# Kernel optimization log

Hardware: AMD Instinct MI355X
Metric: run time of the kernel (lower is better)

Reference implementation:

```python
import jax, jax.numpy as jnp
import numpy as np

NEG_SLOPE = 0.2
EPS = 1e-16


def glorot(key, shape):
    fan = shape[0] + shape[-1] if len(shape) == 2 else shape[-1] * 2
    lim = jnp.sqrt(6.0 / fan)
    return jax.random.uniform(key, shape, minval=-lim, maxval=lim, dtype=jnp.float32)


def setup_inputs() -> dict:
    key = jax.random.key(0)
    ks = jax.random.split(key, 16)
    B, N, E = 4, 50000, 800000
    F_in, H, C, n_cls = 128, 4, 16, 16
    x = jax.random.normal(ks[0], (B, N, F_in), dtype=jnp.float32)
    edge_index = jax.random.randint(ks[1], (2, E), 0, N, dtype=jnp.int64)
    inp = {
        "x": x,
        "edge_index": edge_index,
        # layer 1: 128 -> 4 heads x 16, concat
        "W1": glorot(ks[2], (F_in, H * C)),
        "a1s": glorot(ks[3], (H, C)),
        "a1d": glorot(ks[4], (H, C)),
        "b1": jnp.zeros((H * C,), jnp.float32),
        # layer 2: 64 -> 4 heads x 16, concat
        "W2": glorot(ks[5], (H * C, H * C)),
        "a2s": glorot(ks[6], (H, C)),
        "a2d": glorot(ks[7], (H, C)),
        "b2": jnp.zeros((H * C,), jnp.float32),
        # layer 3: 64 -> 1 head x num_classes, concat
        "W3": glorot(ks[8], (H * C, n_cls)),
        "a3s": glorot(ks[9], (1, n_cls)),
        "a3d": glorot(ks[10], (1, n_cls)),
        "b3": jnp.zeros((n_cls,), jnp.float32),
    }
    return inp


def gat_conv(x, W, a_src, a_dst, b, src, dst, N, concat):
    # x: [N, F_in]; W: [F_in, H*C]
    H, C = a_src.shape
    h = (x @ W).reshape(N, H, C)
    e_src = jnp.einsum('nhc,hc->nh', h, a_src)  # [N, H]
    e_dst = jnp.einsum('nhc,hc->nh', h, a_dst)  # [N, H]
    e = jax.nn.leaky_relu(e_src[src] + e_dst[dst], NEG_SLOPE)  # [E, H]
    # segment softmax over incoming edges of each target node
    m = jax.ops.segment_max(e, dst, num_segments=N)  # [N, H]
    ex = jnp.exp(e - m[dst])
    denom = jax.ops.segment_sum(ex, dst, num_segments=N)  # [N, H]
    alpha = ex / (denom[dst] + EPS)  # [E, H]
    out = jax.ops.segment_sum(alpha[:, :, None] * h[src], dst, num_segments=N)  # [N, H, C]
    out = out.reshape(N, H * C) if concat else out.mean(axis=1)
    return out + b


def reference(x, edge_index, W1, a1s, a1d, b1, W2, a2s, a2d, b2, W3, a3s, a3d, b3):
    B, N, _ = x.shape
    # add self-loops (PyG GATConv default)
    loop = jnp.arange(N, dtype=edge_index.dtype)
    src = jnp.concatenate([edge_index[0], loop])
    dst = jnp.concatenate([edge_index[1], loop])

    def fwd_single(xi):
        h = jax.nn.relu(gat_conv(xi, W1, a1s, a1d, b1, src, dst, N, True))
        h = jax.nn.relu(gat_conv(h, W2, a2s, a2d, b2, src, dst, N, True))
        return gat_conv(h, W3, a3s, a3d, b3, src, dst, N, True)

    return jax.vmap(fwd_single)(x)  # [B, N, num_classes]
```

## Files before the change

kernel.cpp:

```cpp
#include <hip/hip_runtime.h>
#include <hip/hip_bf16.h>
#include <hip/hip_fp16.h>
#include <math.h>


#define NEG_SLOPE 0.2f

constexpr int NN   = 50000;
constexpr int FIN  = 128;
constexpr int HC   = 64;
constexpr int NCLS = 16;

typedef _Float16 half4 __attribute__((ext_vector_type(4)));
typedef float    f32x4 __attribute__((ext_vector_type(4)));

struct H16 { __half2 h[8]; };


__global__ void init_deg_kernel(int* deg, int N) {
    int t = blockIdx.x * blockDim.x + threadIdx.x;
    if (t < N) deg[t] = 1;
}

__global__ void hist_kernel(const int* __restrict__ ei, int* deg, int E) {
    int t = blockIdx.x * blockDim.x + threadIdx.x;
    if (t < E) atomicAdd(&deg[ei[E + t]], 1);
}

__global__ __launch_bounds__(1024) void scan1_kernel(
    const int* __restrict__ deg, int* __restrict__ rp,
    int* __restrict__ bsum, int N) {
    __shared__ int buf[1024];
    int i = blockIdx.x * 1024 + threadIdx.x;
    int v = (i < N) ? deg[i] : 0;
    buf[threadIdx.x] = v;
    __syncthreads();
#pragma unroll
    for (int off = 1; off < 1024; off <<= 1) {
        int t = (threadIdx.x >= (unsigned)off) ? buf[threadIdx.x - off] : 0;
        __syncthreads();
        buf[threadIdx.x] += t;
        __syncthreads();
    }
    if (i < N) rp[i] = buf[threadIdx.x] - v;
    if (threadIdx.x == 1023) bsum[blockIdx.x] = buf[1023];
}

__global__ void scan2_kernel(int* __restrict__ bsum, int nb,
                             int* __restrict__ rp, int N) {
    int lane = threadIdx.x;
    int v = (lane < nb) ? bsum[lane] : 0;
#pragma unroll
    for (int off = 1; off < 64; off <<= 1) {
        int t = __shfl_up(v, off);
        if (lane >= off) v += t;
    }
    if (lane < nb) bsum[lane] = v;
    if (lane == nb - 1) rp[N] = v;
}

__global__ __launch_bounds__(1024) void scan3_kernel(
    int* __restrict__ rp, int* __restrict__ wp,
    const int* __restrict__ bsum, int N) {
    int i = blockIdx.x * 1024 + threadIdx.x;
    if (i >= N) return;
    int add = (blockIdx.x > 0) ? bsum[blockIdx.x - 1] : 0;
    int r = rp[i] + add;
    rp[i] = r;
    wp[i] = r;
}

__global__ void scatter_kernel(const int* __restrict__ ei, int* wp,
                               int* __restrict__ col, int E, int N) {
    int t = blockIdx.x * blockDim.x + threadIdx.x;
    int total = E + N;
    if (t >= total) return;
    if (t < E) {
        int s = ei[t];
        int d = ei[E + t];
        int pos = atomicAdd(&wp[d], 1);
        col[pos] = s;
    } else {
        int n = t - E;
        int pos = atomicAdd(&wp[n], 1);
        col[pos] = n;
    }
}


__global__ void prep_w_kernel(const float* __restrict__ W1,
                              const float* __restrict__ W2,
                              const float* __restrict__ W3,
                              __half* __restrict__ Wt1,
                              __half* __restrict__ Wt2,
                              __half* __restrict__ Wt3) {
    int t = blockIdx.x * 256 + threadIdx.x;
    if (t < 64 * 128) { int c = t >> 7, k = t & 127; Wt1[t] = __float2half(W1[k * 64 + c]); }
    if (t < 64 * 64)  { int c = t >> 6, k = t & 63;  Wt2[t] = __float2half(W2[k * 64 + c]); }
    if (t < 16 * 64)  { int c = t >> 6, k = t & 63;  Wt3[t] = __float2half(W3[k * 16 + c]); }
}


template <int K, int M, int BF, bool IN16>
__global__ __launch_bounds__(256) void gemm_mfma_kernel(
    const void* __restrict__ Xin, const __half* __restrict__ Wt_g,
    const float* __restrict__ as_, const float* __restrict__ ad_,
    __half* __restrict__ Hout, float* __restrict__ Es, float* __restrict__ Ed,
    int N) {
    constexpr int CT = M / 16;
    constexpr int PK = K + 8;
    constexpr int KS = K / 16;
    __shared__ _Float16 Xs[64 * PK];
    __shared__ _Float16 Ws[M * PK];
    const int b = blockIdx.y;
    const int t = threadIdx.x;
    const int node00 = blockIdx.x * 64;

    {
        const float4* wsrc = reinterpret_cast<const float4*>(Wt_g);
        constexpr int WC8 = K / 8;
        for (int idx = t; idx < M * WC8; idx += 256) {
            int c = idx / WC8, kk = idx - c * WC8;
            *reinterpret_cast<float4*>(&Ws[c * PK + kk * 8]) = wsrc[idx];
        }
    }
    if (IN16) {
        const __half* Xh = (const __half*)Xin;
        constexpr int C8 = K / 8;
        for (int idx = t; idx < 64 * C8; idx += 256) {
            int row = idx / C8, k8 = idx - row * C8;
            int node = node00 + row;
            if (node >= N) node = N - 1;
            const float4* src = reinterpret_cast<const float4*>(
                Xh + ((size_t)node * BF + b) * K + k8 * 8);
            *reinterpret_cast<float4*>(&Xs[row * PK + k8 * 8]) = *src;
        }
    } else {
        const float* Xf = (const float*)Xin;
        constexpr int C4 = K / 4;
        for (int idx = t; idx < 64 * C4; idx += 256) {
            int row = idx / C4, k4 = idx - row * C4;
            int node = node00 + row;
            if (node >= N) node = N - 1;
            float4 xv = *reinterpret_cast<const float4*>(
                Xf + ((size_t)b * N + node) * K + k4 * 4);
            half4 hv;
            hv[0] = (_Float16)xv.x; hv[1] = (_Float16)xv.y;
            hv[2] = (_Float16)xv.z; hv[3] = (_Float16)xv.w;
            *reinterpret_cast<half4*>(&Xs[row * PK + k4 * 4]) = hv;
        }
    }
    __syncthreads();

    const int lane = t & 63;
    const int w    = t >> 6;
    const int l15  = lane & 15;
    const int lg   = lane >> 4;
    const int rowb = w * 16;

    f32x4 acc[CT];
#pragma unroll
    for (int ct = 0; ct < CT; ++ct)
#pragma unroll
        for (int r = 0; r < 4; ++r) acc[ct][r] = 0.f;

#pragma unroll
    for (int ks = 0; ks < KS; ++ks) {
        half4 a = *reinterpret_cast<const half4*>(
            &Xs[(rowb + l15) * PK + ks * 16 + lg * 4]);
#pragma unroll
        for (int ct = 0; ct < CT; ++ct) {
            half4 bf = *reinterpret_cast<const half4*>(
                &Ws[(ct * 16 + l15) * PK + ks * 16 + lg * 4]);
            acc[ct] = __builtin_amdgcn_mfma_f32_16x16x16f16(a, bf, acc[ct], 0, 0, 0);
        }
    }

    _Float16* Hh = reinterpret_cast<_Float16*>(Hout);
#pragma unroll
    for (int ct = 0; ct < CT; ++ct) {
        float a_s = as_[ct * 16 + l15];
        float a_d = ad_[ct * 16 + l15];
#pragma unroll
        for (int r = 0; r < 4; ++r) {
            int node = node00 + rowb + lg * 4 + r;
            float hv = acc[ct][r];
            float ps = hv * a_s, pd = hv * a_d;
            ps += __shfl_xor(ps, 1); ps += __shfl_xor(ps, 2);
            ps += __shfl_xor(ps, 4); ps += __shfl_xor(ps, 8);
            pd += __shfl_xor(pd, 1); pd += __shfl_xor(pd, 2);
            pd += __shfl_xor(pd, 4); pd += __shfl_xor(pd, 8);
            if (node < N) {
                Hh[((size_t)node * BF + b) * M + ct * 16 + l15] = (_Float16)hv;
                if (l15 == 0) {
                    Es[((size_t)node * BF + b) * CT + ct] = ps;
                    Ed[((size_t)node * BF + b) * CT + ct] = pd;
                }
            }
        }
    }
}


template <int H, bool RELU, bool OUTB, bool OUTH, int BF>
__global__ __launch_bounds__(256) void agg_kernel(
    const int* __restrict__ rp, const int* __restrict__ col,
    const __half* __restrict__ Hm, const float* __restrict__ Es,
    const float* __restrict__ Ed, const float* __restrict__ bias,
    void* __restrict__ Out, int N) {
    constexpr int C = 16;
    constexpr int M = H * C;
    int t = blockIdx.x * 256 + threadIdx.x;
    if (t >= N * H * BF) return;
    int u = t;
    const int b  = u % BF; u /= BF;
    const int hd = u % H;  u /= H;
    const int n  = u;

    const float ed = Ed[((size_t)n * BF + b) * H + hd];
    const int beg = rp[n], end = rp[n + 1];

    float m = -1e30f, dn = 0.f;
    float acc[C];
#pragma unroll
    for (int j = 0; j < C; ++j) acc[j] = 0.f;

    int i = beg;
    int sA = col[i];
    float esA = Es[((size_t)sA * BF + b) * H + hd];
    H16 hA = *reinterpret_cast<const H16*>(Hm + ((size_t)sA * BF + b) * M + hd * C);

    while (true) {
        int inext = i + 1;
        bool more = (inext < end);
        int sB = 0; float esB = 0.f; H16 hB;
        if (more) {
            sB = col[inext];
            esB = Es[((size_t)sB * BF + b) * H + hd];
            hB = *reinterpret_cast<const H16*>(Hm + ((size_t)sB * BF + b) * M + hd * C);
        }

        float e = esA + ed;
        e = (e >= 0.f) ? e : NEG_SLOPE * e;
        float2 f0 = __half22float2(hA.h[0]);
        float2 f1 = __half22float2(hA.h[1]);
        float2 f2 = __half22float2(hA.h[2]);
        float2 f3 = __half22float2(hA.h[3]);
        float2 f4 = __half22float2(hA.h[4]);
        float2 f5 = __half22float2(hA.h[5]);
        float2 f6 = __half22float2(hA.h[6]);
        float2 f7 = __half22float2(hA.h[7]);
        if (e > m) {
            float sc = __expf(m - e);
            m = e;
            dn = fmaf(dn, sc, 1.0f);
            acc[0]=fmaf(acc[0],sc,f0.x);   acc[1]=fmaf(acc[1],sc,f0.y);
            acc[2]=fmaf(acc[2],sc,f1.x);   acc[3]=fmaf(acc[3],sc,f1.y);
            acc[4]=fmaf(acc[4],sc,f2.x);   acc[5]=fmaf(acc[5],sc,f2.y);
            acc[6]=fmaf(acc[6],sc,f3.x);   acc[7]=fmaf(acc[7],sc,f3.y);
            acc[8]=fmaf(acc[8],sc,f4.x);   acc[9]=fmaf(acc[9],sc,f4.y);
            acc[10]=fmaf(acc[10],sc,f5.x); acc[11]=fmaf(acc[11],sc,f5.y);
            acc[12]=fmaf(acc[12],sc,f6.x); acc[13]=fmaf(acc[13],sc,f6.y);
            acc[14]=fmaf(acc[14],sc,f7.x); acc[15]=fmaf(acc[15],sc,f7.y);
        } else {
            float ex = __expf(e - m);
            dn += ex;
            acc[0]=fmaf(ex,f0.x,acc[0]);   acc[1]=fmaf(ex,f0.y,acc[1]);
            acc[2]=fmaf(ex,f1.x,acc[2]);   acc[3]=fmaf(ex,f1.y,acc[3]);
            acc[4]=fmaf(ex,f2.x,acc[4]);   acc[5]=fmaf(ex,f2.y,acc[5]);
            acc[6]=fmaf(ex,f3.x,acc[6]);   acc[7]=fmaf(ex,f3.y,acc[7]);
            acc[8]=fmaf(ex,f4.x,acc[8]);   acc[9]=fmaf(ex,f4.y,acc[9]);
            acc[10]=fmaf(ex,f5.x,acc[10]); acc[11]=fmaf(ex,f5.y,acc[11]);
            acc[12]=fmaf(ex,f6.x,acc[12]); acc[13]=fmaf(ex,f6.y,acc[13]);
            acc[14]=fmaf(ex,f7.x,acc[14]); acc[15]=fmaf(ex,f7.y,acc[15]);
        }
        if (!more) break;
        i = inext; sA = sB; esA = esB; hA = hB;
    }

    float inv = 1.f / (dn + 1e-16f);
    const float* bp = bias + hd * C;
    float vb[C];
#pragma unroll
    for (int j = 0; j < C; ++j) {
        float v = fmaf(acc[j], inv, bp[j]);
        if (RELU) v = fmaxf(v, 0.f);
        vb[j] = v;
    }
    if (OUTH) {
        __half* op = (__half*)Out + ((size_t)n * BF + b) * M + hd * C;
        H16 hv;
#pragma unroll
        for (int j = 0; j < 8; ++j)
            hv.h[j] = __float22half2_rn(make_float2(vb[2 * j], vb[2 * j + 1]));
        *reinterpret_cast<H16*>(op) = hv;
    } else {
        float* op = OUTB ? ((float*)Out + ((size_t)b * N + n) * M + hd * C)
                         : ((float*)Out + ((size_t)n * BF + b) * M + hd * C);
        *reinterpret_cast<float4*>(op + 0)  = make_float4(vb[0], vb[1], vb[2], vb[3]);
        *reinterpret_cast<float4*>(op + 4)  = make_float4(vb[4], vb[5], vb[6], vb[7]);
        *reinterpret_cast<float4*>(op + 8)  = make_float4(vb[8], vb[9], vb[10], vb[11]);
        *reinterpret_cast<float4*>(op + 12) = make_float4(vb[12], vb[13], vb[14], vb[15]);
    }
}


extern "C" void kernel_launch(void* const* d_in, const int* in_sizes, int n_in,
                              void* d_out, int out_size, void* d_ws, size_t ws_size,
                              hipStream_t stream) {
    const float* x   = (const float*)d_in[0];
    const int*   ei  = (const int*)d_in[1];
    const float* W1  = (const float*)d_in[2];
    const float* a1s = (const float*)d_in[3];
    const float* a1d = (const float*)d_in[4];
    const float* b1  = (const float*)d_in[5];
    const float* W2  = (const float*)d_in[6];
    const float* a2s = (const float*)d_in[7];
    const float* a2d = (const float*)d_in[8];
    const float* b2  = (const float*)d_in[9];
    const float* W3  = (const float*)d_in[10];
    const float* a3s = (const float*)d_in[11];
    const float* a3d = (const float*)d_in[12];
    const float* b3  = (const float*)d_in[13];
    float* outp = (float*)d_out;

    const int N  = NN;
    const int E  = in_sizes[1] / 2;
    const int ET = E + N;
    const int B  = in_sizes[0] / (N * FIN);
    const int NB1024 = (N + 1023) / 1024;

    char* ws = (char*)d_ws;
    size_t off = 0;
    auto alloc = [&](size_t bytes) -> void* {
        void* p = ws + off;
        off += (bytes + 255) & ~(size_t)255;
        return p;
    };
    int* deg  = (int*)alloc((size_t)N * 4);
    int* rp   = (int*)alloc((size_t)(N + 1) * 4);
    int* wp   = (int*)alloc((size_t)N * 4);
    int* bsum = (int*)alloc(64 * 4);
    int* col  = (int*)alloc((size_t)ET * 4);
    __half* Wt1 = (__half*)alloc(64 * 128 * 2);
    __half* Wt2 = (__half*)alloc(64 * 64 * 2);
    __half* Wt3 = (__half*)alloc(16 * 64 * 2);

    size_t fused_need = off + 2 * ((size_t)N * B * HC * 2 + 256)
                            + 2 * ((size_t)N * B * 4 * 4 + 256);
    bool fused = (B == 4) && (ws_size >= fused_need);
    int BF = fused ? 4 : 1;

    __half* h  = (__half*)alloc((size_t)N * BF * HC * 2);
    __half* z  = (__half*)alloc((size_t)N * BF * HC * 2);
    float* es  = (float*)alloc((size_t)N * BF * 4 * 4);
    float* edv = (float*)alloc((size_t)N * BF * 4 * 4);

    init_deg_kernel<<<(N + 255) / 256, 256, 0, stream>>>(deg, N);
    hist_kernel<<<(E + 255) / 256, 256, 0, stream>>>(ei, deg, E);
    scan1_kernel<<<NB1024, 1024, 0, stream>>>(deg, rp, bsum, N);
    scan2_kernel<<<1, 64, 0, stream>>>(bsum, NB1024, rp, N);
    scan3_kernel<<<NB1024, 1024, 0, stream>>>(rp, wp, bsum, N);
    scatter_kernel<<<(ET + 255) / 256, 256, 0, stream>>>(ei, wp, col, E, N);
    prep_w_kernel<<<32, 256, 0, stream>>>(W1, W2, W3, Wt1, Wt2, Wt3);

    if (fused) {
        dim3 g((N + 63) / 64, 4);
        int agg12 = (N * 4 * 4 + 255) / 256;
        int agg3  = (N * 4 + 255) / 256;
        gemm_mfma_kernel<128, 64, 4, false><<<g, 256, 0, stream>>>(x, Wt1, a1s, a1d, h, es, edv, N);
        agg_kernel<4, true, false, true, 4><<<agg12, 256, 0, stream>>>(rp, col, h, es, edv, b1, z, N);
        gemm_mfma_kernel<64, 64, 4, true><<<g, 256, 0, stream>>>(z, Wt2, a2s, a2d, h, es, edv, N);
        agg_kernel<4, true, false, true, 4><<<agg12, 256, 0, stream>>>(rp, col, h, es, edv, b2, z, N);
        gemm_mfma_kernel<64, 16, 4, true><<<g, 256, 0, stream>>>(z, Wt3, a3s, a3d, h, es, edv, N);
        agg_kernel<1, false, true, false, 4><<<agg3, 256, 0, stream>>>(rp, col, h, es, edv, b3, outp, N);
    } else {
        dim3 g((N + 63) / 64, 1);
        int agg12 = (N * 4 + 255) / 256;
        int agg3  = (N + 255) / 256;
        for (int b = 0; b < B; ++b) {
            const float* xb = x + (size_t)b * N * FIN;
            float* outb = outp + (size_t)b * N * NCLS;
            gemm_mfma_kernel<128, 64, 1, false><<<g, 256, 0, stream>>>(xb, Wt1, a1s, a1d, h, es, edv, N);
            agg_kernel<4, true, false, true, 1><<<agg12, 256, 0, stream>>>(rp, col, h, es, edv, b1, z, N);
            gemm_mfma_kernel<64, 64, 1, true><<<g, 256, 0, stream>>>(z, Wt2, a2s, a2d, h, es, edv, N);
            agg_kernel<4, true, false, true, 1><<<agg12, 256, 0, stream>>>(rp, col, h, es, edv, b2, z, N);
            gemm_mfma_kernel<64, 16, 1, true><<<g, 256, 0, stream>>>(z, Wt3, a3s, a3d, h, es, edv, N);
            agg_kernel<1, false, false, false, 1><<<agg3, 256, 0, stream>>>(rp, col, h, es, edv, b3, outb, N);
        }
    }
}
```

Measured before the change: 542.1 us.

## Switch to batch-major layout and split aggregation into 4-channel threads

Intermediate buffers move from node-interleaved batch layout to batch-major layout, so the batch index becomes the outermost dimension. The aggregation kernel now assigns each thread 4 channels of a head instead of all 16, giving 4x more threads, with consecutive threads covering adjacent channel chunks of the same node. Gathers within a batch then touch a smaller working set per batch slice and coalesce across the channel chunks. In exchange, each edge's column index, source score and exp are recomputed by four threads, and cache locality across batches for the same node is lost.

```diff
diff --git a/kernel.cpp b/kernel.cpp
--- a/kernel.cpp
+++ b/kernel.cpp
@@ -14,7 +14,7 @@
 typedef _Float16 half4 __attribute__((ext_vector_type(4)));
 typedef float    f32x4 __attribute__((ext_vector_type(4)));
 
-struct H16 { __half2 h[8]; };
+struct H4v { __half2 h[2]; };
 
 
 __global__ void init_deg_kernel(int* deg, int N) {
@@ -101,7 +101,7 @@
 }
 
 
-template <int K, int M, int BF, bool IN16>
+template <int K, int M, bool IN16>
 __global__ __launch_bounds__(256) void gemm_mfma_kernel(
     const void* __restrict__ Xin, const __half* __restrict__ Wt_g,
     const float* __restrict__ as_, const float* __restrict__ ad_,
@@ -132,7 +132,7 @@
             int node = node00 + row;
             if (node >= N) node = N - 1;
             const float4* src = reinterpret_cast<const float4*>(
-                Xh + ((size_t)node * BF + b) * K + k8 * 8);
+                Xh + ((size_t)b * N + node) * K + k8 * 8);
             *reinterpret_cast<float4*>(&Xs[row * PK + k8 * 8]) = *src;
         }
     } else {
@@ -191,10 +191,10 @@
             pd += __shfl_xor(pd, 1); pd += __shfl_xor(pd, 2);
             pd += __shfl_xor(pd, 4); pd += __shfl_xor(pd, 8);
             if (node < N) {
-                Hh[((size_t)node * BF + b) * M + ct * 16 + l15] = (_Float16)hv;
+                Hh[((size_t)b * N + node) * M + ct * 16 + l15] = (_Float16)hv;
                 if (l15 == 0) {
-                    Es[((size_t)node * BF + b) * CT + ct] = ps;
-                    Ed[((size_t)node * BF + b) * CT + ct] = pd;
+                    Es[((size_t)b * N + node) * CT + ct] = ps;
+                    Ed[((size_t)b * N + node) * CT + ct] = pd;
                 }
             }
         }
@@ -202,105 +202,94 @@
 }
 
 
-template <int H, bool RELU, bool OUTB, bool OUTH, int BF>
+template <int H, bool RELU, bool OUTH, int BF>
 __global__ __launch_bounds__(256) void agg_kernel(
     const int* __restrict__ rp, const int* __restrict__ col,
     const __half* __restrict__ Hm, const float* __restrict__ Es,
     const float* __restrict__ Ed, const float* __restrict__ bias,
     void* __restrict__ Out, int N) {
-    constexpr int C = 16;
-    constexpr int M = H * C;
-    int t = blockIdx.x * 256 + threadIdx.x;
-    if (t >= N * H * BF) return;
-    int u = t;
-    const int b  = u % BF; u /= BF;
-    const int hd = u % H;  u /= H;
-    const int n  = u;
-
-    const float ed = Ed[((size_t)n * BF + b) * H + hd];
+    constexpr int M = H * 16;
+    int g = blockIdx.x * 256 + threadIdx.x;
+    int n, b, hd, ch;
+    if (H == 4) {
+        if (g >= N * 16 * BF) return;
+        b = (BF > 1) ? g / (N * 16) : 0;
+        int r = (BF > 1) ? g % (N * 16) : g;
+        n = r >> 4;
+        int q = r & 15;
+        hd = q >> 2;
+        ch = q & 3;
+    } else {
+        if (g >= N * 4 * BF) return;
+        n = g / (4 * BF);
+        int q = g % (4 * BF);
+        b = (BF > 1) ? (q >> 2) : 0;
+        ch = q & 3;
+        hd = 0;
+    }
+    const int c0 = hd * 16 + ch * 4;
+    const size_t tb = (size_t)b * N;
+
+    const float ed = Ed[(tb + n) * H + hd];
     const int beg = rp[n], end = rp[n + 1];
 
     float m = -1e30f, dn = 0.f;
-    float acc[C];
-#pragma unroll
-    for (int j = 0; j < C; ++j) acc[j] = 0.f;
+    float a0 = 0.f, a1 = 0.f, a2 = 0.f, a3 = 0.f;
 
     int i = beg;
     int sA = col[i];
-    float esA = Es[((size_t)sA * BF + b) * H + hd];
-    H16 hA = *reinterpret_cast<const H16*>(Hm + ((size_t)sA * BF + b) * M + hd * C);
+    float esA = Es[(tb + sA) * H + hd];
+    H4v hA = *reinterpret_cast<const H4v*>(Hm + (tb + sA) * M + c0);
 
     while (true) {
         int inext = i + 1;
         bool more = (inext < end);
-        int sB = 0; float esB = 0.f; H16 hB;
+        int sB = 0; float esB = 0.f; H4v hB;
         if (more) {
             sB = col[inext];
-            esB = Es[((size_t)sB * BF + b) * H + hd];
-            hB = *reinterpret_cast<const H16*>(Hm + ((size_t)sB * BF + b) * M + hd * C);
+            esB = Es[(tb + sB) * H + hd];
+            hB = *reinterpret_cast<const H4v*>(Hm + (tb + sB) * M + c0);
         }
 
         float e = esA + ed;
         e = (e >= 0.f) ? e : NEG_SLOPE * e;
         float2 f0 = __half22float2(hA.h[0]);
         float2 f1 = __half22float2(hA.h[1]);
-        float2 f2 = __half22float2(hA.h[2]);
-        float2 f3 = __half22float2(hA.h[3]);
-        float2 f4 = __half22float2(hA.h[4]);
-        float2 f5 = __half22float2(hA.h[5]);
-        float2 f6 = __half22float2(hA.h[6]);
-        float2 f7 = __half22float2(hA.h[7]);
         if (e > m) {
             float sc = __expf(m - e);
             m = e;
             dn = fmaf(dn, sc, 1.0f);
-            acc[0]=fmaf(acc[0],sc,f0.x);   acc[1]=fmaf(acc[1],sc,f0.y);
-            acc[2]=fmaf(acc[2],sc,f1.x);   acc[3]=fmaf(acc[3],sc,f1.y);
-            acc[4]=fmaf(acc[4],sc,f2.x);   acc[5]=fmaf(acc[5],sc,f2.y);
-            acc[6]=fmaf(acc[6],sc,f3.x);   acc[7]=fmaf(acc[7],sc,f3.y);
-            acc[8]=fmaf(acc[8],sc,f4.x);   acc[9]=fmaf(acc[9],sc,f4.y);
-            acc[10]=fmaf(acc[10],sc,f5.x); acc[11]=fmaf(acc[11],sc,f5.y);
-            acc[12]=fmaf(acc[12],sc,f6.x); acc[13]=fmaf(acc[13],sc,f6.y);
-            acc[14]=fmaf(acc[14],sc,f7.x); acc[15]=fmaf(acc[15],sc,f7.y);
+            a0 = fmaf(a0, sc, f0.x); a1 = fmaf(a1, sc, f0.y);
+            a2 = fmaf(a2, sc, f1.x); a3 = fmaf(a3, sc, f1.y);
         } else {
             float ex = __expf(e - m);
             dn += ex;
-            acc[0]=fmaf(ex,f0.x,acc[0]);   acc[1]=fmaf(ex,f0.y,acc[1]);
-            acc[2]=fmaf(ex,f1.x,acc[2]);   acc[3]=fmaf(ex,f1.y,acc[3]);
-            acc[4]=fmaf(ex,f2.x,acc[4]);   acc[5]=fmaf(ex,f2.y,acc[5]);
-            acc[6]=fmaf(ex,f3.x,acc[6]);   acc[7]=fmaf(ex,f3.y,acc[7]);
-            acc[8]=fmaf(ex,f4.x,acc[8]);   acc[9]=fmaf(ex,f4.y,acc[9]);
-            acc[10]=fmaf(ex,f5.x,acc[10]); acc[11]=fmaf(ex,f5.y,acc[11]);
-            acc[12]=fmaf(ex,f6.x,acc[12]); acc[13]=fmaf(ex,f6.y,acc[13]);
-            acc[14]=fmaf(ex,f7.x,acc[14]); acc[15]=fmaf(ex,f7.y,acc[15]);
+            a0 = fmaf(ex, f0.x, a0); a1 = fmaf(ex, f0.y, a1);
+            a2 = fmaf(ex, f1.x, a2); a3 = fmaf(ex, f1.y, a3);
         }
         if (!more) break;
         i = inext; sA = sB; esA = esB; hA = hB;
     }
 
     float inv = 1.f / (dn + 1e-16f);
-    const float* bp = bias + hd * C;
-    float vb[C];
-#pragma unroll
-    for (int j = 0; j < C; ++j) {
-        float v = fmaf(acc[j], inv, bp[j]);
-        if (RELU) v = fmaxf(v, 0.f);
-        vb[j] = v;
+    const float* bp = bias + c0;
+    float v0 = fmaf(a0, inv, bp[0]);
+    float v1 = fmaf(a1, inv, bp[1]);
+    float v2 = fmaf(a2, inv, bp[2]);
+    float v3 = fmaf(a3, inv, bp[3]);
+    if (RELU) {
+        v0 = fmaxf(v0, 0.f); v1 = fmaxf(v1, 0.f);
+        v2 = fmaxf(v2, 0.f); v3 = fmaxf(v3, 0.f);
     }
     if (OUTH) {
-        __half* op = (__half*)Out + ((size_t)n * BF + b) * M + hd * C;
-        H16 hv;
-#pragma unroll
-        for (int j = 0; j < 8; ++j)
-            hv.h[j] = __float22half2_rn(make_float2(vb[2 * j], vb[2 * j + 1]));
-        *reinterpret_cast<H16*>(op) = hv;
-    } else {
-        float* op = OUTB ? ((float*)Out + ((size_t)b * N + n) * M + hd * C)
-                         : ((float*)Out + ((size_t)n * BF + b) * M + hd * C);
-        *reinterpret_cast<float4*>(op + 0)  = make_float4(vb[0], vb[1], vb[2], vb[3]);
-        *reinterpret_cast<float4*>(op + 4)  = make_float4(vb[4], vb[5], vb[6], vb[7]);
-        *reinterpret_cast<float4*>(op + 8)  = make_float4(vb[8], vb[9], vb[10], vb[11]);
-        *reinterpret_cast<float4*>(op + 12) = make_float4(vb[12], vb[13], vb[14], vb[15]);
+        __half* op = (__half*)Out + (tb + n) * M + c0;
+        H4v hv;
+        hv.h[0] = __float22half2_rn(make_float2(v0, v1));
+        hv.h[1] = __float22half2_rn(make_float2(v2, v3));
+        *reinterpret_cast<H4v*>(op) = hv;
+    } else {
+        float* op = (float*)Out + (tb + n) * M + c0;
+        *reinterpret_cast<float4*>(op) = make_float4(v0, v1, v2, v3);
     }
 }
 
@@ -349,12 +338,6 @@
     size_t fused_need = off + 2 * ((size_t)N * B * HC * 2 + 256)
                             + 2 * ((size_t)N * B * 4 * 4 + 256);
     bool fused = (B == 4) && (ws_size >= fused_need);
-    int BF = fused ? 4 : 1;
-
-    __half* h  = (__half*)alloc((size_t)N * BF * HC * 2);
-    __half* z  = (__half*)alloc((size_t)N * BF * HC * 2);
-    float* es  = (float*)alloc((size_t)N * BF * 4 * 4);
-    float* edv = (float*)alloc((size_t)N * BF * 4 * 4);
 
     init_deg_kernel<<<(N + 255) / 256, 256, 0, stream>>>(deg, N);
     hist_kernel<<<(E + 255) / 256, 256, 0, stream>>>(ei, deg, E);
@@ -365,28 +348,36 @@
     prep_w_kernel<<<32, 256, 0, stream>>>(W1, W2, W3, Wt1, Wt2, Wt3);
 
     if (fused) {
+        __half* h  = (__half*)alloc((size_t)N * B * HC * 2);
+        __half* z  = (__half*)alloc((size_t)N * B * HC * 2);
+        float* es  = (float*)alloc((size_t)N * B * 4 * 4);
+        float* edv = (float*)alloc((size_t)N * B * 4 * 4);
         dim3 g((N + 63) / 64, 4);
-        int agg12 = (N * 4 * 4 + 255) / 256;
+        int agg12 = (N * 16 * 4 + 255) / 256;
+        int agg3  = (N * 4 * 4 + 255) / 256;
+        gemm_mfma_kernel<128, 64, false><<<g, 256, 0, stream>>>(x, Wt1, a1s, a1d, h, es, edv, N);
+        agg_kernel<4, true, true, 4><<<agg12, 256, 0, stream>>>(rp, col, h, es, edv, b1, z, N);
+        gemm_mfma_kernel<64, 64, true><<<g, 256, 0, stream>>>(z, Wt2, a2s, a2d, h, es, edv, N);
+        agg_kernel<4, true, true, 4><<<agg12, 256, 0, stream>>>(rp, col, h, es, edv, b2, z, N);
+        gemm_mfma_kernel<64, 16, true><<<g, 256, 0, stream>>>(z, Wt3, a3s, a3d, h, es, edv, N);
+        agg_kernel<1, false, false, 4><<<agg3, 256, 0, stream>>>(rp, col, h, es, edv, b3, outp, N);
+    } else {
+        __half* h  = (__half*)alloc((size_t)N * HC * 2);
+        __half* z  = (__half*)alloc((size_t)N * HC * 2);
+        float* es  = (float*)alloc((size_t)N * 4 * 4);
+        float* edv = (float*)alloc((size_t)N * 4 * 4);
+        dim3 g((N + 63) / 64, 1);
+        int agg12 = (N * 16 + 255) / 256;
         int agg3  = (N * 4 + 255) / 256;
-        gemm_mfma_kernel<128, 64, 4, false><<<g, 256, 0, stream>>>(x, Wt1, a1s, a1d, h, es, edv, N);
-        agg_kernel<4, true, false, true, 4><<<agg12, 256, 0, stream>>>(rp, col, h, es, edv, b1, z, N);
-        gemm_mfma_kernel<64, 64, 4, true><<<g, 256, 0, stream>>>(z, Wt2, a2s, a2d, h, es, edv, N);
-        agg_kernel<4, true, false, true, 4><<<agg12, 256, 0, stream>>>(rp, col, h, es, edv, b2, z, N);
-        gemm_mfma_kernel<64, 16, 4, true><<<g, 256, 0, stream>>>(z, Wt3, a3s, a3d, h, es, edv, N);
-        agg_kernel<1, false, true, false, 4><<<agg3, 256, 0, stream>>>(rp, col, h, es, edv, b3, outp, N);
-    } else {
-        dim3 g((N + 63) / 64, 1);
-        int agg12 = (N * 4 + 255) / 256;
-        int agg3  = (N + 255) / 256;
         for (int b = 0; b < B; ++b) {
             const float* xb = x + (size_t)b * N * FIN;
             float* outb = outp + (size_t)b * N * NCLS;
-            gemm_mfma_kernel<128, 64, 1, false><<<g, 256, 0, stream>>>(xb, Wt1, a1s, a1d, h, es, edv, N);
-            agg_kernel<4, true, false, true, 1><<<agg12, 256, 0, stream>>>(rp, col, h, es, edv, b1, z, N);
-            gemm_mfma_kernel<64, 64, 1, true><<<g, 256, 0, stream>>>(z, Wt2, a2s, a2d, h, es, edv, N);
-            agg_kernel<4, true, false, true, 1><<<agg12, 256, 0, stream>>>(rp, col, h, es, edv, b2, z, N);
-            gemm_mfma_kernel<64, 16, 1, true><<<g, 256, 0, stream>>>(z, Wt3, a3s, a3d, h, es, edv, N);
-            agg_kernel<1, false, false, false, 1><<<agg3, 256, 0, stream>>>(rp, col, h, es, edv, b3, outb, N);
-        }
-    }
-}
+            gemm_mfma_kernel<128, 64, false><<<g, 256, 0, stream>>>(xb, Wt1, a1s, a1d, h, es, edv, N);
+            agg_kernel<4, true, true, 1><<<agg12, 256, 0, stream>>>(rp, col, h, es, edv, b1, z, N);
+            gemm_mfma_kernel<64, 64, true><<<g, 256, 0, stream>>>(z, Wt2, a2s, a2d, h, es, edv, N);
+            agg_kernel<4, true, true, 1><<<agg12, 256, 0, stream>>>(rp, col, h, es, edv, b2, z, N);
+            gemm_mfma_kernel<64, 16, true><<<g, 256, 0, stream>>>(z, Wt3, a3s, a3d, h, es, edv, N);
+            agg_kernel<1, false, false, 1><<<agg3, 256, 0, stream>>>(rp, col, h, es, edv, b3, outb, N);
+        }
+    }
+}
```

After: 645.7 us. 19.1% more time.

## Switch fused intermediates from node-interleaved to batch-major layout

Applied to the files above, without the earlier changes.

Stores per-layer features and attention scores as [batch][node] instead of [node][batch], and remaps aggregation threads so batch is the outermost index. Each group of threads then gathers neighbor rows from a single batch's smaller slice. The aim is better cache locality for the random neighbor gathers. The cost is losing the coalescing of the four batches of one source node into one contiguous 128-byte read.

```diff
diff --git a/kernel.cpp b/kernel.cpp
--- a/kernel.cpp
+++ b/kernel.cpp
@@ -101,7 +101,7 @@
 }
 
 
-template <int K, int M, int BF, bool IN16>
+template <int K, int M, bool IN16>
 __global__ __launch_bounds__(256) void gemm_mfma_kernel(
     const void* __restrict__ Xin, const __half* __restrict__ Wt_g,
     const float* __restrict__ as_, const float* __restrict__ ad_,
@@ -132,7 +132,7 @@
             int node = node00 + row;
             if (node >= N) node = N - 1;
             const float4* src = reinterpret_cast<const float4*>(
-                Xh + ((size_t)node * BF + b) * K + k8 * 8);
+                Xh + ((size_t)b * N + node) * K + k8 * 8);
             *reinterpret_cast<float4*>(&Xs[row * PK + k8 * 8]) = *src;
         }
     } else {
@@ -191,10 +191,10 @@
             pd += __shfl_xor(pd, 1); pd += __shfl_xor(pd, 2);
             pd += __shfl_xor(pd, 4); pd += __shfl_xor(pd, 8);
             if (node < N) {
-                Hh[((size_t)node * BF + b) * M + ct * 16 + l15] = (_Float16)hv;
+                Hh[((size_t)b * N + node) * M + ct * 16 + l15] = (_Float16)hv;
                 if (l15 == 0) {
-                    Es[((size_t)node * BF + b) * CT + ct] = ps;
-                    Ed[((size_t)node * BF + b) * CT + ct] = pd;
+                    Es[((size_t)b * N + node) * CT + ct] = ps;
+                    Ed[((size_t)b * N + node) * CT + ct] = pd;
                 }
             }
         }
@@ -202,7 +202,7 @@
 }
 
 
-template <int H, bool RELU, bool OUTB, bool OUTH, int BF>
+template <int H, bool RELU, bool OUTH, int BF>
 __global__ __launch_bounds__(256) void agg_kernel(
     const int* __restrict__ rp, const int* __restrict__ col,
     const __half* __restrict__ Hm, const float* __restrict__ Es,
@@ -210,14 +210,22 @@
     void* __restrict__ Out, int N) {
     constexpr int C = 16;
     constexpr int M = H * C;
-    int t = blockIdx.x * 256 + threadIdx.x;
-    if (t >= N * H * BF) return;
-    int u = t;
-    const int b  = u % BF; u /= BF;
-    const int hd = u % H;  u /= H;
-    const int n  = u;
-
-    const float ed = Ed[((size_t)n * BF + b) * H + hd];
+    int g = blockIdx.x * 256 + threadIdx.x;
+    if (g >= N * H * BF) return;
+    int b, n, hd;
+    if (H == 4) {
+        b = (BF > 1) ? g / (N * 4) : 0;
+        int r = (BF > 1) ? g % (N * 4) : g;
+        n = r >> 2;
+        hd = r & 3;
+    } else {
+        b = (BF > 1) ? g / N : 0;
+        n = (BF > 1) ? g % N : g;
+        hd = 0;
+    }
+    const size_t tb = (size_t)b * N;
+
+    const float ed = Ed[(tb + n) * H + hd];
     const int beg = rp[n], end = rp[n + 1];
 
     float m = -1e30f, dn = 0.f;
@@ -227,8 +235,8 @@
 
     int i = beg;
     int sA = col[i];
-    float esA = Es[((size_t)sA * BF + b) * H + hd];
-    H16 hA = *reinterpret_cast<const H16*>(Hm + ((size_t)sA * BF + b) * M + hd * C);
+    float esA = Es[(tb + sA) * H + hd];
+    H16 hA = *reinterpret_cast<const H16*>(Hm + (tb + sA) * M + hd * C);
 
     while (true) {
         int inext = i + 1;
@@ -236,8 +244,8 @@
         int sB = 0; float esB = 0.f; H16 hB;
         if (more) {
             sB = col[inext];
-            esB = Es[((size_t)sB * BF + b) * H + hd];
-            hB = *reinterpret_cast<const H16*>(Hm + ((size_t)sB * BF + b) * M + hd * C);
+            esB = Es[(tb + sB) * H + hd];
+            hB = *reinterpret_cast<const H16*>(Hm + (tb + sB) * M + hd * C);
         }
 
         float e = esA + ed;
@@ -288,15 +296,14 @@
         vb[j] = v;
     }
     if (OUTH) {
-        __half* op = (__half*)Out + ((size_t)n * BF + b) * M + hd * C;
+        __half* op = (__half*)Out + (tb + n) * M + hd * C;
         H16 hv;
 #pragma unroll
         for (int j = 0; j < 8; ++j)
             hv.h[j] = __float22half2_rn(make_float2(vb[2 * j], vb[2 * j + 1]));
         *reinterpret_cast<H16*>(op) = hv;
     } else {
-        float* op = OUTB ? ((float*)Out + ((size_t)b * N + n) * M + hd * C)
-                         : ((float*)Out + ((size_t)n * BF + b) * M + hd * C);
+        float* op = (float*)Out + (tb + n) * M + hd * C;
         *reinterpret_cast<float4*>(op + 0)  = make_float4(vb[0], vb[1], vb[2], vb[3]);
         *reinterpret_cast<float4*>(op + 4)  = make_float4(vb[4], vb[5], vb[6], vb[7]);
         *reinterpret_cast<float4*>(op + 8)  = make_float4(vb[8], vb[9], vb[10], vb[11]);
@@ -349,12 +356,6 @@
     size_t fused_need = off + 2 * ((size_t)N * B * HC * 2 + 256)
                             + 2 * ((size_t)N * B * 4 * 4 + 256);
     bool fused = (B == 4) && (ws_size >= fused_need);
-    int BF = fused ? 4 : 1;
-
-    __half* h  = (__half*)alloc((size_t)N * BF * HC * 2);
-    __half* z  = (__half*)alloc((size_t)N * BF * HC * 2);
-    float* es  = (float*)alloc((size_t)N * BF * 4 * 4);
-    float* edv = (float*)alloc((size_t)N * BF * 4 * 4);
 
     init_deg_kernel<<<(N + 255) / 256, 256, 0, stream>>>(deg, N);
     hist_kernel<<<(E + 255) / 256, 256, 0, stream>>>(ei, deg, E);
@@ -365,28 +366,36 @@
     prep_w_kernel<<<32, 256, 0, stream>>>(W1, W2, W3, Wt1, Wt2, Wt3);
 
     if (fused) {
+        __half* h  = (__half*)alloc((size_t)N * B * HC * 2);
+        __half* z  = (__half*)alloc((size_t)N * B * HC * 2);
+        float* es  = (float*)alloc((size_t)N * B * 4 * 4);
+        float* edv = (float*)alloc((size_t)N * B * 4 * 4);
         dim3 g((N + 63) / 64, 4);
         int agg12 = (N * 4 * 4 + 255) / 256;
         int agg3  = (N * 4 + 255) / 256;
-        gemm_mfma_kernel<128, 64, 4, false><<<g, 256, 0, stream>>>(x, Wt1, a1s, a1d, h, es, edv, N);
-        agg_kernel<4, true, false, true, 4><<<agg12, 256, 0, stream>>>(rp, col, h, es, edv, b1, z, N);
-        gemm_mfma_kernel<64, 64, 4, true><<<g, 256, 0, stream>>>(z, Wt2, a2s, a2d, h, es, edv, N);
-        agg_kernel<4, true, false, true, 4><<<agg12, 256, 0, stream>>>(rp, col, h, es, edv, b2, z, N);
-        gemm_mfma_kernel<64, 16, 4, true><<<g, 256, 0, stream>>>(z, Wt3, a3s, a3d, h, es, edv, N);
-        agg_kernel<1, false, true, false, 4><<<agg3, 256, 0, stream>>>(rp, col, h, es, edv, b3, outp, N);
+        gemm_mfma_kernel<128, 64, false><<<g, 256, 0, stream>>>(x, Wt1, a1s, a1d, h, es, edv, N);
+        agg_kernel<4, true, true, 4><<<agg12, 256, 0, stream>>>(rp, col, h, es, edv, b1, z, N);
+        gemm_mfma_kernel<64, 64, true><<<g, 256, 0, stream>>>(z, Wt2, a2s, a2d, h, es, edv, N);
+        agg_kernel<4, true, true, 4><<<agg12, 256, 0, stream>>>(rp, col, h, es, edv, b2, z, N);
+        gemm_mfma_kernel<64, 16, true><<<g, 256, 0, stream>>>(z, Wt3, a3s, a3d, h, es, edv, N);
+        agg_kernel<1, false, false, 4><<<agg3, 256, 0, stream>>>(rp, col, h, es, edv, b3, outp, N);
     } else {
+        __half* h  = (__half*)alloc((size_t)N * HC * 2);
+        __half* z  = (__half*)alloc((size_t)N * HC * 2);
+        float* es  = (float*)alloc((size_t)N * 4 * 4);
+        float* edv = (float*)alloc((size_t)N * 4 * 4);
         dim3 g((N + 63) / 64, 1);
         int agg12 = (N * 4 + 255) / 256;
         int agg3  = (N + 255) / 256;
         for (int b = 0; b < B; ++b) {
             const float* xb = x + (size_t)b * N * FIN;
             float* outb = outp + (size_t)b * N * NCLS;
-            gemm_mfma_kernel<128, 64, 1, false><<<g, 256, 0, stream>>>(xb, Wt1, a1s, a1d, h, es, edv, N);
-            agg_kernel<4, true, false, true, 1><<<agg12, 256, 0, stream>>>(rp, col, h, es, edv, b1, z, N);
-            gemm_mfma_kernel<64, 64, 1, true><<<g, 256, 0, stream>>>(z, Wt2, a2s, a2d, h, es, edv, N);
-            agg_kernel<4, true, false, true, 1><<<agg12, 256, 0, stream>>>(rp, col, h, es, edv, b2, z, N);
-            gemm_mfma_kernel<64, 16, 1, true><<<g, 256, 0, stream>>>(z, Wt3, a3s, a3d, h, es, edv, N);
-            agg_kernel<1, false, false, false, 1><<<agg3, 256, 0, stream>>>(rp, col, h, es, edv, b3, outb, N);
-        }
-    }
-}
+            gemm_mfma_kernel<128, 64, false><<<g, 256, 0, stream>>>(xb, Wt1, a1s, a1d, h, es, edv, N);
+            agg_kernel<4, true, true, 1><<<agg12, 256, 0, stream>>>(rp, col, h, es, edv, b1, z, N);
+            gemm_mfma_kernel<64, 64, true><<<g, 256, 0, stream>>>(z, Wt2, a2s, a2d, h, es, edv, N);
+            agg_kernel<4, true, true, 1><<<agg12, 256, 0, stream>>>(rp, col, h, es, edv, b2, z, N);
+            gemm_mfma_kernel<64, 16, true><<<g, 256, 0, stream>>>(z, Wt3, a3s, a3d, h, es, edv, N);
+            agg_kernel<1, false, false, 1><<<agg3, 256, 0, stream>>>(rp, col, h, es, edv, b3, outb, N);
+        }
+    }
+}
```

New measurement: 609.3 us. +12.4%, slower.
